# Kernel optimization log

Measured on AMD Instinct MI355X. Metric: run time of the kernel, lower is better.

The kernel has to match this reference:

```python
import jax, jax.numpy as jnp
import numpy as np
import math

DIM = 1024
NUM_HEADS = 16
HEAD_DIM = DIM // NUM_HEADS  # 64
BATCH = 4
SEQ = 4096


def setup_inputs() -> dict:
    key = jax.random.key(0)
    ks = jax.random.split(key, 10)
    s = 1.0 / math.sqrt(DIM)
    return {
        "x": jax.random.normal(ks[0], (BATCH, SEQ, DIM), dtype=jnp.float32),
        "Wq": jax.random.normal(ks[1], (DIM, DIM), dtype=jnp.float32) * s,
        "bq": jax.random.normal(ks[2], (DIM,), dtype=jnp.float32) * 0.01,
        "Wk": jax.random.normal(ks[3], (DIM, DIM), dtype=jnp.float32) * s,
        "bk": jax.random.normal(ks[4], (DIM,), dtype=jnp.float32) * 0.01,
        "Wv": jax.random.normal(ks[5], (DIM, DIM), dtype=jnp.float32) * s,
        "bv": jax.random.normal(ks[6], (DIM,), dtype=jnp.float32) * 0.01,
        "Wo": jax.random.normal(ks[7], (DIM, DIM), dtype=jnp.float32) * s,
        "bo": jax.random.normal(ks[8], (DIM,), dtype=jnp.float32) * 0.01,
        # Performer random projection buffer: randn * 0.4, [head_dim, feature_map_size]
        "R": jax.random.normal(ks[9], (HEAD_DIM, HEAD_DIM), dtype=jnp.float32) * 0.4,
    }


def _feature_map(x, R):
    # x: [b, h, n, d]; matches torch: x scaled first, then norm of scaled x
    x = x / math.sqrt(HEAD_DIM)
    proj = jnp.einsum("bhnd,dm->bhnm", x, R)
    sq_norm = jnp.sum(x * x, axis=-1, keepdims=True)  # ||x||^2
    return jnp.exp(proj - 0.5 * sq_norm)


def reference(x, Wq, bq, Wk, bk, Wv, bv, Wo, bo, R):
    b, n, _ = x.shape
    h, d = NUM_HEADS, HEAD_DIM

    def split_heads(t):
        return t.reshape(b, n, h, d).transpose(0, 2, 1, 3)  # [b,h,n,d]

    q = split_heads(x @ Wq.T + bq)
    k = split_heads(x @ Wk.T + bk)
    v = split_heads(x @ Wv.T + bv)

    q_prime = _feature_map(q, R)  # [b,h,n,m]
    k_prime = _feature_map(k, R)  # [b,h,n,m]

    kv = jnp.einsum("bhnd,bhne->bhde", k_prime, v)          # [b,h,m,d]
    z = 1.0 / (jnp.sum(q_prime, axis=-1) + 1e-8)            # [b,h,n]
    out = jnp.einsum("bhnd,bhde,bhn->bhne", q_prime, kv, z)  # [b,h,n,d]

    out = out.transpose(0, 2, 1, 3).reshape(b, n, DIM)
    return out @ Wo.T + bo
```

## Files before the change

### kernel.cpp

```cpp
#include <hip/hip_runtime.h>
#include <math.h>

#define DIM 1024
#define NH 16
#define HD 64
#define BATCH 4
#define SEQ 4096
#define NTOK (BATCH*SEQ)

typedef float f32x4 __attribute__((ext_vector_type(4)));
typedef short bf16x8 __attribute__((ext_vector_type(8)));

#define GLOAD_LDS16(gp, lp)                                                    \
  __builtin_amdgcn_global_load_lds(                                            \
      (const __attribute__((address_space(1))) unsigned int*)(gp),             \
      (__attribute__((address_space(3))) unsigned int*)(lp), 16, 0, 0)

__device__ __forceinline__ unsigned short f2bf(float f) {
  unsigned u = __float_as_uint(f);
  unsigned r = (u + 0x7fffu + ((u >> 16) & 1u)) >> 16;
  return (unsigned short)r;
}
__device__ __forceinline__ float bf2f(unsigned short s) {
  return __uint_as_float((unsigned)s << 16);
}

template <int NT_N, int OUT_BF16>
__global__ __launch_bounds__(512, 2) void gemm256(
    const unsigned short* __restrict__ A,
    const unsigned short* __restrict__ B,
    const float* __restrict__ b0, const float* __restrict__ b1,
    const float* __restrict__ b2,
    void* __restrict__ C0, void* __restrict__ C1, void* __restrict__ C2)
{
    __shared__ unsigned short lds[4][2][8192];
    const int t    = threadIdx.x;
    const int lane = t & 63;
    const int w    = t >> 6;

    const int cpx = gridDim.x >> 3;
    const int swz = (blockIdx.x & 7) * cpx + (blockIdx.x >> 3);
    const int mi  = swz / NT_N;
    const int ni  = swz % NT_N;
    const int m0  = mi * 256;
    const int n0g = ni * 256;

    const int wm = (w >> 2) * 128;
    const int wn = (w & 3) * 64;

    const int srow = t >> 2;
    const int sseg = ((t & 3) ^ ((t >> 3) & 3)) * 8;
    const unsigned short* Ag = A + (size_t)(m0 + srow) * 1024 + sseg;
    const unsigned short* Bg = B + (size_t)(n0g + srow) * 1024 + sseg;
    const int ldst = w * 512;

    const int fr = lane & 15;
    const int fq = ((lane >> 4) ^ ((fr >> 1) & 3)) * 8;

    f32x4 acc[8][4] = {};

#define STAGE_A(hh, j)                                                        \
  GLOAD_LDS16(Ag + (size_t)(j) * 131072 + (size_t)(hh) * 32,                  \
              &lds[(hh) & 3][0][(j) * 4096 + ldst])
#define STAGE_B(hh, j)                                                        \
  GLOAD_LDS16(Bg + (size_t)(j) * 131072 + (size_t)(hh) * 32,                  \
              &lds[(hh) & 3][1][(j) * 4096 + ldst])

#define BOUNDARY(VM)                                                          \
  asm volatile("s_waitcnt vmcnt(" #VM ")" ::: "memory");                      \
  __builtin_amdgcn_s_barrier();                                               \
  asm volatile("" ::: "memory");

#define KHALF(h, DOSTAGE)                                                     \
  {                                                                           \
    const unsigned short* As_ = &lds[(h) & 3][0][0];                          \
    const unsigned short* Bs_ = &lds[(h) & 3][1][0];                          \
    bf16x8 bfr[4], afr[4];                                                    \
    if (DOSTAGE) { STAGE_A((h) + 3, 0); STAGE_A((h) + 3, 1); }                \
    _Pragma("unroll")                                                         \
    for (int nf = 0; nf < 4; ++nf)                                            \
      bfr[nf] = *(const bf16x8*)&Bs_[(wn + nf * 16 + fr) * 32 + fq];          \
    _Pragma("unroll")                                                         \
    for (int mf = 0; mf < 4; ++mf)                                            \
      afr[mf] = *(const bf16x8*)&As_[(wm + mf * 16 + fr) * 32 + fq];          \
    __builtin_amdgcn_s_barrier();                                             \
    asm volatile("s_waitcnt lgkmcnt(0)" ::: "memory");                        \
    __builtin_amdgcn_s_setprio(1);                                            \
    _Pragma("unroll")                                                         \
    for (int mf = 0; mf < 4; ++mf)                                            \
      _Pragma("unroll")                                                       \
      for (int nf = 0; nf < 4; ++nf)                                          \
        acc[mf][nf] = __builtin_amdgcn_mfma_f32_16x16x32_bf16(                \
            afr[mf], bfr[nf], acc[mf][nf], 0, 0, 0);                          \
    __builtin_amdgcn_s_setprio(0);                                            \
    __builtin_amdgcn_s_barrier();                                             \
    asm volatile("" ::: "memory");                                            \
    if (DOSTAGE) { STAGE_B((h) + 3, 0); STAGE_B((h) + 3, 1); }                \
    _Pragma("unroll")                                                         \
    for (int mf = 0; mf < 4; ++mf)                                            \
      afr[mf] = *(const bf16x8*)&As_[(wm + 64 + mf * 16 + fr) * 32 + fq];     \
    __builtin_amdgcn_s_barrier();                                             \
    asm volatile("s_waitcnt lgkmcnt(0)" ::: "memory");                        \
    __builtin_amdgcn_s_setprio(1);                                            \
    _Pragma("unroll")                                                         \
    for (int mf = 0; mf < 4; ++mf)                                            \
      _Pragma("unroll")                                                       \
      for (int nf = 0; nf < 4; ++nf)                                          \
        acc[4 + mf][nf] = __builtin_amdgcn_mfma_f32_16x16x32_bf16(            \
            afr[mf], bfr[nf], acc[4 + mf][nf], 0, 0, 0);                      \
    __builtin_amdgcn_s_setprio(0);                                            \
  }

#pragma unroll
    for (int hh = 0; hh < 3; ++hh) {
        STAGE_A(hh, 0); STAGE_A(hh, 1);
        STAGE_B(hh, 0); STAGE_B(hh, 1);
    }

#pragma unroll 1
    for (int h = 0; h < 29; ++h) {
        BOUNDARY(8);
        KHALF(h, 1);
    }
    BOUNDARY(8); KHALF(29, 0);
    BOUNDARY(4); KHALF(30, 0);
    BOUNDARY(0); KHALF(31, 0);

#undef KHALF
#undef BOUNDARY
#undef STAGE_A
#undef STAGE_B

    const int mat = ni >> 2;
    const float* bias = (mat == 0) ? b0 : (mat == 1) ? b1 : b2;
    void* Cp = (mat == 0) ? C0 : (mat == 1) ? C1 : C2;
    const int n0 = (ni & 3) * 256;

    const int col = lane & 15;
    const int rq  = (lane >> 4) * 4;
#pragma unroll
    for (int nf = 0; nf < 4; ++nf) {
        int cbase = n0 + wn + nf * 16 + col;
        float bv = bias[cbase];
#pragma unroll
        for (int mf = 0; mf < 8; ++mf) {
            int rbase = m0 + wm + (mf >> 2) * 64 + (mf & 3) * 16 + rq;
#pragma unroll
            for (int r = 0; r < 4; ++r) {
                float val = acc[mf][nf][r] + bv;
                size_t idx = (size_t)(rbase + r) * 1024 + cbase;
                if (OUT_BF16)
                    ((unsigned short*)Cp)[idx] = f2bf(val);
                else
                    ((float*)Cp)[idx] = val;
            }
        }
    }
}

__global__ __launch_bounds__(256) void cast_bf16(
    const float* __restrict__ src, unsigned short* __restrict__ dst, int n)
{
    int i = (blockIdx.x * 256 + threadIdx.x) * 4;
    if (i >= n) return;
    float4 v = *(const float4*)&src[i];
    ushort2 lo = {f2bf(v.x), f2bf(v.y)};
    ushort2 hi = {f2bf(v.z), f2bf(v.w)};
    *(ushort2*)&dst[i] = lo;
    *(ushort2*)&dst[i + 2] = hi;
}

__global__ __launch_bounds__(256) void cast_bf16_w4(
    const float* __restrict__ s0, const float* __restrict__ s1,
    const float* __restrict__ s2, const float* __restrict__ s3,
    unsigned short* __restrict__ d0, unsigned short* __restrict__ d1,
    unsigned short* __restrict__ d2, unsigned short* __restrict__ d3)
{
    const float* s = (blockIdx.y == 0) ? s0 : (blockIdx.y == 1) ? s1
                    : (blockIdx.y == 2) ? s2 : s3;
    unsigned short* d = (blockIdx.y == 0) ? d0 : (blockIdx.y == 1) ? d1
                       : (blockIdx.y == 2) ? d2 : d3;
    int i = (blockIdx.x * 256 + threadIdx.x) * 4;
    float4 v = *(const float4*)&s[i];
    ushort2 lo = {f2bf(v.x), f2bf(v.y)};
    ushort2 hi = {f2bf(v.z), f2bf(v.w)};
    *(ushort2*)&d[i] = lo;
    *(ushort2*)&d[i + 2] = hi;
}

__global__ __launch_bounds__(256) void featmap_mfma(
    unsigned short* __restrict__ buf, const float* __restrict__ R)
{
    __shared__ unsigned short Rt[64 * 72];
    const int t = threadIdx.x;
    for (int i = t; i < 4096; i += 256) {
        int n = i >> 6, k = i & 63;
        Rt[n * 72 + k] = f2bf(R[k * 64 + n]);
    }
    __syncthreads();

    const int lane = t & 63;
    const int w = t >> 6;
    const size_t rowbase = (size_t)blockIdx.x * 256 + w * 64;
    const int fr = lane & 15;
    const int fq = (lane >> 4) * 8;

    f32x4 acc[4][4] = {};
    float sqacc[4] = {0.f, 0.f, 0.f, 0.f};

#pragma unroll
    for (int ks = 0; ks < 2; ks++) {
        bf16x8 bfr[4];
#pragma unroll
        for (int nt = 0; nt < 4; nt++)
            bfr[nt] = *(const bf16x8*)&Rt[(nt * 16 + fr) * 72 + ks * 32 + fq];
#pragma unroll
        for (int mt = 0; mt < 4; mt++) {
            bf16x8 a = *(const bf16x8*)
                &buf[(rowbase + mt * 16 + fr) * 64 + ks * 32 + fq];
#pragma unroll
            for (int j = 0; j < 8; j++) {
                float v = bf2f((unsigned short)a[j]);
                sqacc[mt] = fmaf(v, v, sqacc[mt]);
            }
#pragma unroll
            for (int nt = 0; nt < 4; nt++)
                acc[mt][nt] = __builtin_amdgcn_mfma_f32_16x16x32_bf16(
                    a, bfr[nt], acc[mt][nt], 0, 0, 0);
        }
    }
#pragma unroll
    for (int mt = 0; mt < 4; mt++) {
        sqacc[mt] += __shfl_xor(sqacc[mt], 16);
        sqacc[mt] += __shfl_xor(sqacc[mt], 32);
    }

    const int col = lane & 15;
    const int rq  = (lane >> 4) * 4;
#pragma unroll
    for (int mt = 0; mt < 4; mt++) {
#pragma unroll
        for (int r = 0; r < 4; r++) {
            float s = __shfl(sqacc[mt], rq + r);
            size_t row = rowbase + mt * 16 + rq + r;
#pragma unroll
            for (int nt = 0; nt < 4; nt++) {
                float val = acc[mt][nt][r] * 0.125f - s * 0.0078125f;
                buf[row * 64 + nt * 16 + col] = f2bf(__expf(val));
            }
        }
    }
}

__global__ __launch_bounds__(256) void kv_accum(
    const unsigned short* __restrict__ kp, const unsigned short* __restrict__ vp,
    float* __restrict__ kv)
{
    __shared__ float Ks[16][68];
    __shared__ float Vs[16][68];
    const int chunk = blockIdx.x;
    const int h = blockIdx.y;
    const int b = blockIdx.z;
    const int t = threadIdx.x;
    const int tx = t & 15, ty = t >> 4;
    float c[4][4] = {};
    const int nbase = b * SEQ + chunk * 512;
    const int nl = t >> 4, seg = t & 15;
    for (int n0 = 0; n0 < 512; n0 += 16) {
        size_t gaddr = (size_t)(nbase + n0 + nl) * DIM + h * 64 + seg * 4;
        ushort4 kq = *(const ushort4*)&kp[gaddr];
        ushort4 vq = *(const ushort4*)&vp[gaddr];
        Ks[nl][seg * 4 + 0] = bf2f(kq.x); Ks[nl][seg * 4 + 1] = bf2f(kq.y);
        Ks[nl][seg * 4 + 2] = bf2f(kq.z); Ks[nl][seg * 4 + 3] = bf2f(kq.w);
        Vs[nl][seg * 4 + 0] = bf2f(vq.x); Vs[nl][seg * 4 + 1] = bf2f(vq.y);
        Vs[nl][seg * 4 + 2] = bf2f(vq.z); Vs[nl][seg * 4 + 3] = bf2f(vq.w);
        __syncthreads();
#pragma unroll
        for (int nn = 0; nn < 16; nn++) {
            float4 a = *(const float4*)&Ks[nn][ty * 4];
            float4 bq = *(const float4*)&Vs[nn][tx * 4];
            float aa[4] = {a.x, a.y, a.z, a.w};
            float bb[4] = {bq.x, bq.y, bq.z, bq.w};
#pragma unroll
            for (int i = 0; i < 4; i++)
#pragma unroll
                for (int j = 0; j < 4; j++)
                    c[i][j] += aa[i] * bb[j];
        }
        __syncthreads();
    }
    float* dst = &kv[(size_t)(b * NH + h) * 64 * 64];
#pragma unroll
    for (int i = 0; i < 4; i++)
#pragma unroll
        for (int j = 0; j < 4; j++)
            atomicAdd(&dst[(ty * 4 + i) * 64 + tx * 4 + j], c[i][j]);
}

__global__ __launch_bounds__(256) void attn_out_mfma(
    const unsigned short* __restrict__ qp, const float* __restrict__ kv,
    unsigned short* __restrict__ ob)
{
    __shared__ unsigned short kvT[64 * 72];
    const int t = threadIdx.x;
    const int bh = blockIdx.y;
    const int b = bh >> 4, h = bh & 15;
    const float* kvp = &kv[(size_t)bh * 4096];
    for (int i = t; i < 4096; i += 256) {
        int m = i >> 6, e = i & 63;
        kvT[e * 72 + m] = f2bf(kvp[i]);
    }
    __syncthreads();

    const int lane = t & 63;
    const int w = t >> 6;
    const int rowInSeq = blockIdx.x * 256 + w * 64;
    const int fr = lane & 15;
    const int fq = (lane >> 4) * 8;

    f32x4 acc[4][4] = {};
    float rsum[4] = {0.f, 0.f, 0.f, 0.f};

#pragma unroll
    for (int ks = 0; ks < 2; ks++) {
        bf16x8 bfr[4];
#pragma unroll
        for (int nt = 0; nt < 4; nt++)
            bfr[nt] = *(const bf16x8*)&kvT[(nt * 16 + fr) * 72 + ks * 32 + fq];
#pragma unroll
        for (int mt = 0; mt < 4; mt++) {
            size_t n = (size_t)(b * SEQ + rowInSeq + mt * 16 + fr);
            bf16x8 a = *(const bf16x8*)&qp[n * DIM + h * 64 + ks * 32 + fq];
#pragma unroll
            for (int j = 0; j < 8; j++)
                rsum[mt] += bf2f((unsigned short)a[j]);
#pragma unroll
            for (int nt = 0; nt < 4; nt++)
                acc[mt][nt] = __builtin_amdgcn_mfma_f32_16x16x32_bf16(
                    a, bfr[nt], acc[mt][nt], 0, 0, 0);
        }
    }
#pragma unroll
    for (int mt = 0; mt < 4; mt++) {
        rsum[mt] += __shfl_xor(rsum[mt], 16);
        rsum[mt] += __shfl_xor(rsum[mt], 32);
    }

    const int col = lane & 15;
    const int rq  = (lane >> 4) * 4;
#pragma unroll
    for (int mt = 0; mt < 4; mt++) {
#pragma unroll
        for (int r = 0; r < 4; r++) {
            float s = __shfl(rsum[mt], rq + r);
            float z = 1.f / (s + 1e-8f);
            size_t n = (size_t)(b * SEQ + rowInSeq + mt * 16 + rq + r);
#pragma unroll
            for (int nt = 0; nt < 4; nt++)
                ob[n * DIM + h * 64 + nt * 16 + col] = f2bf(acc[mt][nt][r] * z);
        }
    }
}

extern "C" void kernel_launch(void* const* d_in, const int* in_sizes, int n_in,
                              void* d_out, int out_size, void* d_ws, size_t ws_size,
                              hipStream_t stream) {
    const float* x  = (const float*)d_in[0];
    const float* Wq = (const float*)d_in[1];
    const float* bq = (const float*)d_in[2];
    const float* Wk = (const float*)d_in[3];
    const float* bk = (const float*)d_in[4];
    const float* Wv = (const float*)d_in[5];
    const float* bv = (const float*)d_in[6];
    const float* Wo = (const float*)d_in[7];
    const float* bo = (const float*)d_in[8];
    const float* R  = (const float*)d_in[9];
    float* out = (float*)d_out;

    char* p = (char*)d_ws;
    unsigned short* xb = (unsigned short*)p; p += (size_t)NTOK * DIM * 2;
    unsigned short* qb = (unsigned short*)p; p += (size_t)NTOK * DIM * 2;
    unsigned short* kb = (unsigned short*)p; p += (size_t)NTOK * DIM * 2;
    unsigned short* vb = (unsigned short*)p; p += (size_t)NTOK * DIM * 2;
    float* kvb = (float*)p;                  p += (size_t)BATCH * NH * HD * HD * 4;
    unsigned short* wqkv = (unsigned short*)p; p += (size_t)3 * DIM * DIM * 2;
    unsigned short* wob  = (unsigned short*)p; p += (size_t)DIM * DIM * 2;

    hipMemsetAsync(kvb, 0, (size_t)BATCH * NH * HD * HD * sizeof(float), stream);

    cast_bf16<<<NTOK * DIM / (256 * 4), 256, 0, stream>>>(x, xb, NTOK * DIM);
    cast_bf16_w4<<<dim3(DIM * DIM / (256 * 4), 4), 256, 0, stream>>>(
        Wq, Wk, Wv, Wo,
        wqkv, wqkv + (size_t)DIM * DIM, wqkv + (size_t)2 * DIM * DIM, wob);

    gemm256<12, 1><<<768, 512, 0, stream>>>(
        xb, wqkv, bq, bk, bv, qb, kb, vb);

    featmap_mfma<<<2 * NTOK * NH / 256, 256, 0, stream>>>(qb, R);

    kv_accum<<<dim3(8, NH, BATCH), 256, 0, stream>>>(kb, vb, kvb);

    attn_out_mfma<<<dim3(SEQ / 256, BATCH * NH), 256, 0, stream>>>(qb, kvb, xb);

    gemm256<4, 0><<<256, 512, 0, stream>>>(
        xb, wob, bo, bo, bo, out, out, out);
}
```

Baseline: 415.6 us.

## Software-pipeline LDS fragment loads across k-steps in GEMM main loop

Restructures the GEMM main loop so that the B fragments and first A fragments for the next k-step are read from LDS at the end of the current step, double-buffering B fragments in registers. It also staggers the A and B global-to-LDS staging at different points in the step and fully unrolls all 32 steps. The aim is to hide LDS read latency behind MFMA work and cut the number of barriers per step. The cost is higher register pressure and code size, and the new buffer-reuse ordering carries race risk.

After: 426.9 us. +2.7%, slower.

```diff
diff --git a/kernel.cpp b/kernel.cpp
--- a/kernel.cpp
+++ b/kernel.cpp
@@ -33,7 +33,8 @@
     const float* __restrict__ b2,
     void* __restrict__ C0, void* __restrict__ C1, void* __restrict__ C2)
 {
-    __shared__ unsigned short lds[4][2][8192];
+    __shared__ unsigned short SA[4][8192];
+    __shared__ unsigned short SB[4][8192];
     const int t    = threadIdx.x;
     const int lane = t & 63;
     const int w    = t >> 6;
@@ -58,78 +59,109 @@
     const int fq = ((lane >> 4) ^ ((fr >> 1) & 3)) * 8;
 
     f32x4 acc[8][4] = {};
-
-#define STAGE_A(hh, j)                                                        \
-  GLOAD_LDS16(Ag + (size_t)(j) * 131072 + (size_t)(hh) * 32,                  \
-              &lds[(hh) & 3][0][(j) * 4096 + ldst])
-#define STAGE_B(hh, j)                                                        \
-  GLOAD_LDS16(Bg + (size_t)(j) * 131072 + (size_t)(hh) * 32,                  \
-              &lds[(hh) & 3][1][(j) * 4096 + ldst])
-
-#define BOUNDARY(VM)                                                          \
-  asm volatile("s_waitcnt vmcnt(" #VM ")" ::: "memory");                      \
+    bf16x8 a1[4], a2[4], bb[2][4];
+
+#define STGA(k, j)                                                            \
+  GLOAD_LDS16(Ag + (size_t)(j) * 131072 + (size_t)(k) * 32,                   \
+              &SA[(k) & 3][(j) * 4096 + ldst])
+#define STGB(k, j)                                                            \
+  GLOAD_LDS16(Bg + (size_t)(j) * 131072 + (size_t)(k) * 32,                   \
+              &SB[(k) & 3][(j) * 4096 + ldst])
+#define VMW_(N) asm volatile("s_waitcnt vmcnt(" #N ")" ::: "memory")
+#define VMW(N) VMW_(N)
+#define MEMFENCE asm volatile("" ::: "memory")
+#define BARRIER                                                               \
   __builtin_amdgcn_s_barrier();                                               \
-  asm volatile("" ::: "memory");
-
-#define KHALF(h, DOSTAGE)                                                     \
+  __builtin_amdgcn_sched_barrier(0)
+
+#define BODY(h, VM)                                                           \
   {                                                                           \
-    const unsigned short* As_ = &lds[(h) & 3][0][0];                          \
-    const unsigned short* Bs_ = &lds[(h) & 3][1][0];                          \
-    bf16x8 bfr[4], afr[4];                                                    \
-    if (DOSTAGE) { STAGE_A((h) + 3, 0); STAGE_A((h) + 3, 1); }                \
-    _Pragma("unroll")                                                         \
-    for (int nf = 0; nf < 4; ++nf)                                            \
-      bfr[nf] = *(const bf16x8*)&Bs_[(wn + nf * 16 + fr) * 32 + fq];          \
-    _Pragma("unroll")                                                         \
-    for (int mf = 0; mf < 4; ++mf)                                            \
-      afr[mf] = *(const bf16x8*)&As_[(wm + mf * 16 + fr) * 32 + fq];          \
-    __builtin_amdgcn_s_barrier();                                             \
-    asm volatile("s_waitcnt lgkmcnt(0)" ::: "memory");                        \
     __builtin_amdgcn_s_setprio(1);                                            \
     _Pragma("unroll")                                                         \
     for (int mf = 0; mf < 4; ++mf)                                            \
       _Pragma("unroll")                                                       \
       for (int nf = 0; nf < 4; ++nf)                                          \
         acc[mf][nf] = __builtin_amdgcn_mfma_f32_16x16x32_bf16(                \
-            afr[mf], bfr[nf], acc[mf][nf], 0, 0, 0);                          \
+            a1[mf], bb[(h) & 1][nf], acc[mf][nf], 0, 0, 0);                   \
     __builtin_amdgcn_s_setprio(0);                                            \
-    __builtin_amdgcn_s_barrier();                                             \
-    asm volatile("" ::: "memory");                                            \
-    if (DOSTAGE) { STAGE_B((h) + 3, 0); STAGE_B((h) + 3, 1); }                \
+    if ((h) <= 28) { STGB((h) + 3, 0); STGB((h) + 3, 1); }                    \
     _Pragma("unroll")                                                         \
     for (int mf = 0; mf < 4; ++mf)                                            \
-      afr[mf] = *(const bf16x8*)&As_[(wm + 64 + mf * 16 + fr) * 32 + fq];     \
-    __builtin_amdgcn_s_barrier();                                             \
-    asm volatile("s_waitcnt lgkmcnt(0)" ::: "memory");                        \
+      a2[mf] = *(const bf16x8*)                                               \
+          &SA[(h) & 3][(wm + 64 + mf * 16 + fr) * 32 + fq];                   \
+    VMW(VM);                                                                  \
+    BARRIER;                                                                  \
     __builtin_amdgcn_s_setprio(1);                                            \
     _Pragma("unroll")                                                         \
     for (int mf = 0; mf < 4; ++mf)                                            \
       _Pragma("unroll")                                                       \
       for (int nf = 0; nf < 4; ++nf)                                          \
         acc[4 + mf][nf] = __builtin_amdgcn_mfma_f32_16x16x32_bf16(            \
-            afr[mf], bfr[nf], acc[4 + mf][nf], 0, 0, 0);                      \
+            a2[mf], bb[(h) & 1][nf], acc[4 + mf][nf], 0, 0, 0);               \
     __builtin_amdgcn_s_setprio(0);                                            \
+    if ((h) <= 27) { STGA((h) + 4, 0); STGA((h) + 4, 1); }                    \
+    _Pragma("unroll")                                                         \
+    for (int nf = 0; nf < 4; ++nf)                                            \
+      bb[((h) + 1) & 1][nf] = *(const bf16x8*)                                \
+          &SB[((h) + 1) & 3][(wn + nf * 16 + fr) * 32 + fq];                  \
+    _Pragma("unroll")                                                         \
+    for (int mf = 0; mf < 4; ++mf)                                            \
+      a1[mf] = *(const bf16x8*)                                               \
+          &SA[((h) + 1) & 3][(wm + mf * 16 + fr) * 32 + fq];                  \
+    MEMFENCE;                                                                 \
+    BARRIER;                                                                  \
   }
 
-#pragma unroll
-    for (int hh = 0; hh < 3; ++hh) {
-        STAGE_A(hh, 0); STAGE_A(hh, 1);
-        STAGE_B(hh, 0); STAGE_B(hh, 1);
-    }
-
-#pragma unroll 1
-    for (int h = 0; h < 29; ++h) {
-        BOUNDARY(8);
-        KHALF(h, 1);
-    }
-    BOUNDARY(8); KHALF(29, 0);
-    BOUNDARY(4); KHALF(30, 0);
-    BOUNDARY(0); KHALF(31, 0);
-
-#undef KHALF
-#undef BOUNDARY
-#undef STAGE_A
-#undef STAGE_B
+    STGA(0, 0); STGA(0, 1); STGB(0, 0); STGB(0, 1);
+    STGA(1, 0); STGA(1, 1); STGB(1, 0); STGB(1, 1);
+    STGA(2, 0); STGA(2, 1); STGB(2, 0); STGB(2, 1);
+    VMW(8);
+    BARRIER;
+    STGA(3, 0); STGA(3, 1);
+#pragma unroll
+    for (int nf = 0; nf < 4; ++nf)
+        bb[0][nf] = *(const bf16x8*)&SB[0][(wn + nf * 16 + fr) * 32 + fq];
+#pragma unroll
+    for (int mf = 0; mf < 4; ++mf)
+        a1[mf] = *(const bf16x8*)&SA[0][(wm + mf * 16 + fr) * 32 + fq];
+    MEMFENCE;
+    BARRIER;
+
+    BODY(0, 8)  BODY(1, 8)  BODY(2, 8)  BODY(3, 8)  BODY(4, 8)
+    BODY(5, 8)  BODY(6, 8)  BODY(7, 8)  BODY(8, 8)  BODY(9, 8)
+    BODY(10, 8) BODY(11, 8) BODY(12, 8) BODY(13, 8) BODY(14, 8)
+    BODY(15, 8) BODY(16, 8) BODY(17, 8) BODY(18, 8) BODY(19, 8)
+    BODY(20, 8) BODY(21, 8) BODY(22, 8) BODY(23, 8) BODY(24, 8)
+    BODY(25, 8) BODY(26, 8) BODY(27, 8) BODY(28, 8)
+    BODY(29, 4) BODY(30, 0)
+
+    __builtin_amdgcn_s_setprio(1);
+#pragma unroll
+    for (int mf = 0; mf < 4; ++mf)
+#pragma unroll
+        for (int nf = 0; nf < 4; ++nf)
+            acc[mf][nf] = __builtin_amdgcn_mfma_f32_16x16x32_bf16(
+                a1[mf], bb[1][nf], acc[mf][nf], 0, 0, 0);
+    __builtin_amdgcn_s_setprio(0);
+#pragma unroll
+    for (int mf = 0; mf < 4; ++mf)
+        a2[mf] = *(const bf16x8*)&SA[3][(wm + 64 + mf * 16 + fr) * 32 + fq];
+    __builtin_amdgcn_s_setprio(1);
+#pragma unroll
+    for (int mf = 0; mf < 4; ++mf)
+#pragma unroll
+        for (int nf = 0; nf < 4; ++nf)
+            acc[4 + mf][nf] = __builtin_amdgcn_mfma_f32_16x16x32_bf16(
+                a2[mf], bb[1][nf], acc[4 + mf][nf], 0, 0, 0);
+    __builtin_amdgcn_s_setprio(0);
+
+#undef BODY
+#undef BARRIER
+#undef MEMFENCE
+#undef VMW
+#undef VMW_
+#undef STGB
+#undef STGA
 
     const int mat = ni >> 2;
     const float* bias = (mat == 0) ? b0 : (mat == 1) ? b1 : b2;
```
